# Kernel optimization log

Hardware: AMD Instinct MI355X
Metric: run time of the kernel (lower is better)

## Reference

```python
import jax, jax.numpy as jnp
import numpy as np

C = 1024
CI = 256  # in_channels // inter_ratio
BN_EPS = 1e-5


def setup_inputs() -> dict:
    key = jax.random.key(0)
    ks = jax.random.split(key, 12)
    B, H, W = 16, 64, 32
    xavier = lambda k, o, i: jax.random.uniform(k, (o, i), jnp.float32,
                                                -np.sqrt(6.0 / (o + i)), np.sqrt(6.0 / (o + i)))
    return {
        "x": jax.random.normal(ks[0], (B, C, H, W), jnp.float32),
        "theta_w": xavier(ks[1], CI, C), "theta_b": jnp.zeros((CI,), jnp.float32),
        "phi_w": xavier(ks[2], CI, C), "phi_b": jnp.zeros((CI,), jnp.float32),
        "g_w": xavier(ks[3], CI, C), "g_b": jnp.zeros((CI,), jnp.float32),
        "w_w": xavier(ks[4], C, CI), "w_b": jnp.zeros((C,), jnp.float32),
        # BatchNorm (inference-mode) params; random (not zero-init) so the block is non-trivial
        "bn_gamma": jax.random.normal(ks[5], (C,), jnp.float32) * 0.1 + 1.0,
        "bn_beta": jax.random.normal(ks[6], (C,), jnp.float32) * 0.1,
        "bn_mean": jax.random.normal(ks[7], (C,), jnp.float32) * 0.1,
        "bn_var": jax.random.uniform(ks[8], (C,), jnp.float32, 0.5, 1.5),
    }


def reference(x, theta_w, theta_b, phi_w, phi_b, g_w, g_b, w_w, w_b,
              bn_gamma, bn_beta, bn_mean, bn_var):
    B, Cc, H, W = x.shape
    N = H * W
    xf = x.reshape(B, Cc, N)  # [B, C, N]
    # 1x1 convs == channel GEMMs
    theta = jnp.einsum('oc,bcn->bno', theta_w, xf) + theta_b  # [B, N, Ci]
    phi = jnp.einsum('oc,bcn->bon', phi_w, xf) + phi_b[:, None]  # [B, Ci, N]
    g = jnp.einsum('oc,bcn->bno', g_w, xf) + g_b  # [B, N, Ci]
    attn = jax.nn.softmax(jnp.einsum('bno,bom->bnm', theta, phi), axis=-1)  # [B, N, N]
    y = jnp.einsum('bnm,bmo->bno', attn, g)  # [B, N, Ci]
    z = jnp.einsum('co,bno->bcn', w_w, y) + w_b[None, :, None]  # [B, C, N]
    inv = bn_gamma / jnp.sqrt(bn_var + BN_EPS)
    z = (z - bn_mean[None, :, None]) * inv[None, :, None] + bn_beta[None, :, None]
    return z.reshape(B, Cc, H, W) + x
```

## Files before the change

### kernel.cpp

```cpp
#include <hip/hip_runtime.h>
#include <cstdint>

#define BATCH 16
#define CH 1024
#define CIN 256
#define NSP 2048
#define BN_EPS 1e-5f

typedef _Float16 f16;
typedef f16   f16x8 __attribute__((ext_vector_type(8)));
typedef float f32x4 __attribute__((ext_vector_type(4)));

typedef __attribute__((address_space(3))) void lds_t;
typedef __attribute__((address_space(1))) const void gbl_t;

__device__ __forceinline__ void gld16(void* l, const void* g) {
    __builtin_amdgcn_global_load_lds((gbl_t*)g, (lds_t*)l, 16, 0, 0);
}

__global__ __launch_bounds__(256) void k_prep(
    const float* __restrict__ tw, const float* __restrict__ pw,
    const float* __restrict__ gw, const float* __restrict__ ww,
    const float* __restrict__ wb, const float* __restrict__ gamma,
    const float* __restrict__ beta, const float* __restrict__ mean,
    const float* __restrict__ var,
    f16* __restrict__ w_all, float* __restrict__ inv_out, float* __restrict__ off_out)
{
    int id = blockIdx.x * 256 + threadIdx.x;
    if (id < 4 * 262144) {
        int sel = id >> 18, off = id & 262143;
        const float* src = sel == 0 ? tw : sel == 1 ? pw : sel == 2 ? gw : ww;
        w_all[id] = (f16)src[off];
    } else {
        int c = id - 4 * 262144;
        if (c < CH) {
            float iv = gamma[c] * rsqrtf(var[c] + BN_EPS);
            inv_out[c] = iv;
            off_out[c] = (wb[c] - mean[c]) * iv + beta[c];
        }
    }
}

__global__ __launch_bounds__(256) void k_transpose_x(
    const float* __restrict__ x, f16* __restrict__ xT)
{
    __shared__ float tile[64 * 65];
    int t = threadIdx.x;
    int n0 = blockIdx.x * 64, c0 = blockIdx.y * 64, b = blockIdx.z;
    const float* xb = x + (size_t)b * CH * NSP;
    for (int k = 0; k < 4; ++k) {
        int id = t + 256 * k;
        int row = id >> 4, cc = id & 15;
        float4 v = *(const float4*)(xb + (size_t)(c0 + row) * NSP + n0 + cc * 4);
        tile[row * 65 + cc * 4 + 0] = v.x;
        tile[row * 65 + cc * 4 + 1] = v.y;
        tile[row * 65 + cc * 4 + 2] = v.z;
        tile[row * 65 + cc * 4 + 3] = v.w;
    }
    __syncthreads();
    f16* xTb = xT + (size_t)b * NSP * CH;
    for (int k = 0; k < 2; ++k) {
        int id = t + 256 * k;
        int n = id >> 3, c8 = id & 7;
        f16x8 o;
        #pragma unroll
        for (int j = 0; j < 8; ++j) o[j] = (f16)tile[(c8 * 8 + j) * 65 + n];
        *(f16x8*)(xTb + (size_t)(n0 + n) * CH + c0 + c8 * 8) = o;
    }
}

__global__ __launch_bounds__(256, 3) void k_qkv(
    const f16* __restrict__ xT, const f16* __restrict__ w_all,
    const float* __restrict__ tb, const float* __restrict__ pb,
    const float* __restrict__ gb,
    f16* __restrict__ theta, f16* __restrict__ phiT, f16* __restrict__ gT)
{
    __shared__ char smem[40960];
    f16* a_lds = (f16*)smem;
    f16* b_lds = (f16*)(smem + 8192);
    int t = threadIdx.x;
    int w = t >> 6, lane = t & 63, l15 = lane & 15, q = lane >> 4;
    int sw = l15 & 7;
    int n0 = blockIdx.x * 64, b = blockIdx.y, set = blockIdx.z;
    const f16* W  = w_all + (size_t)set * (CIN * CH);
    const f16* xA = xT + ((size_t)b * NSP + n0) * CH;

    int rA  = lane >> 3;
    int ccs = (lane & 7) ^ rA;

    f32x4 acc[4][4];
    #pragma unroll
    for (int i = 0; i < 4; ++i)
        #pragma unroll
        for (int j = 0; j < 4; ++j) acc[i][j] = (f32x4){0.f, 0.f, 0.f, 0.f};

    for (int it = 0; it < 16; ++it) {
        #pragma unroll
        for (int i = 0; i < 2; ++i) {
            int win = w * 2 + i;
            int n = win * 8 + rA;
            gld16((char*)a_lds + win * 1024,
                  xA + (size_t)n * CH + it * 64 + ccs * 8);
        }
        #pragma unroll
        for (int i = 0; i < 8; ++i) {
            int win = w * 8 + i;
            int o = win * 8 + rA;
            gld16((char*)b_lds + win * 1024,
                  W + (size_t)o * CH + it * 64 + ccs * 8);
        }
        __syncthreads();

        #pragma unroll
        for (int kl = 0; kl < 2; ++kl) {
            int c16 = kl * 4 + q;
            int pos = (c16 ^ sw) & 7;
            f16x8 af[4], bfr[4];
            #pragma unroll
            for (int tn = 0; tn < 4; ++tn)
                af[tn] = *(const f16x8*)(a_lds + (16 * tn + l15) * 64 + pos * 8);
            #pragma unroll
            for (int to = 0; to < 4; ++to)
                bfr[to] = *(const f16x8*)(b_lds + (64 * w + 16 * to + l15) * 64 + pos * 8);
            #pragma unroll
            for (int tn = 0; tn < 4; ++tn)
                #pragma unroll
                for (int to = 0; to < 4; ++to)
                    acc[tn][to] = __builtin_amdgcn_mfma_f32_16x16x32_f16(
                        af[tn], bfr[to], acc[tn][to], 0, 0, 0);
        }
        __syncthreads();
    }

    const float* bias = set == 0 ? tb : set == 1 ? pb : gb;
    float bv[4];
    #pragma unroll
    for (int to = 0; to < 4; ++to) bv[to] = bias[64 * w + 16 * to + l15];

    if (set < 2) {
        f16* e_lds = (f16*)smem;
        #pragma unroll
        for (int tn = 0; tn < 4; ++tn)
            #pragma unroll
            for (int to = 0; to < 4; ++to)
                #pragma unroll
                for (int r = 0; r < 4; ++r)
                    e_lds[(16 * tn + 4 * q + r) * 256 + 64 * w + 16 * to + l15] =
                        (f16)(acc[tn][to][r] + bv[to]);
        __syncthreads();
        f16* dst = (set == 0 ? theta : phiT) + ((size_t)b * NSP + n0) * CIN;
        for (int k2 = 0; k2 < 8; ++k2) {
            int id = t + 256 * k2;
            *(f16x8*)(dst + id * 8) = *(const f16x8*)(e_lds + id * 8);
        }
    } else {
        f16* e_lds = (f16*)smem;
        #pragma unroll
        for (int tn = 0; tn < 4; ++tn)
            #pragma unroll
            for (int to = 0; to < 4; ++to)
                #pragma unroll
                for (int r = 0; r < 4; ++r)
                    e_lds[(64 * w + 16 * to + l15) * 72 + 16 * tn + 4 * q + r] =
                        (f16)(acc[tn][to][r] + bv[to]);
        __syncthreads();
        f16* dst = gT + (size_t)b * CIN * NSP + n0;
        for (int k2 = 0; k2 < 8; ++k2) {
            int id = t + 256 * k2;
            int o = id >> 3, cc = id & 7;
            *(f16x8*)(dst + (size_t)o * NSP + cc * 8) = *(const f16x8*)(e_lds + o * 72 + cc * 8);
        }
    }
}

__global__ __launch_bounds__(256, 2) void k_attn(
    const f16* __restrict__ theta, const f16* __restrict__ phiT,
    const f16* __restrict__ gT, f16* __restrict__ y)
{
    __shared__ char smem[70656];
    f16* p_lds = (f16*)(smem + 65536);
    int t = threadIdx.x;
    int w = t >> 6, lane = t & 63, l15 = lane & 15, q = lane >> 4;
    int n0 = blockIdx.x * 64, b = blockIdx.y;

    f16x8 th[8];
    const f16* thp = theta + ((size_t)b * NSP + n0 + 16 * w + l15) * CIN + q * 8;
    #pragma unroll
    for (int kk = 0; kk < 8; ++kk) th[kk] = *(const f16x8*)(thp + kk * 32);

    f32x4 yacc[16];
    #pragma unroll
    for (int i = 0; i < 16; ++i) yacc[i] = (f32x4){0.f, 0.f, 0.f, 0.f};
    float m_run = -INFINITY, l_run = 0.f;

    const f16* phib = phiT + (size_t)b * NSP * CIN;
    const f16* gTb  = gT + (size_t)b * CIN * NSP;

    int prow_in = lane >> 5;
    int pchunk  = lane & 31;
    int grow_in = lane >> 2;
    int gslot   = lane & 3;

    auto stage = [&](int it, int bufsel) {
        char* pbuf = smem + bufsel * 16384;
        char* gbuf = smem + 32768 + bufsel * 16384;
        const f16* psrc = phib + (size_t)(it * 32) * CIN;
        #pragma unroll
        for (int i = 0; i < 4; ++i) {
            int win = w * 4 + i;
            int row = win * 2 + prow_in;
            int c = (pchunk & 24) | ((pchunk ^ row) & 7);
            gld16(pbuf + win * 1024, psrc + (size_t)row * CIN + c * 8);
        }
        #pragma unroll
        for (int i = 0; i < 4; ++i) {
            int win = w * 4 + i;
            int o = win * 16 + grow_in;
            int c = (gslot ^ o) & 3;
            gld16(gbuf + win * 1024, gTb + (size_t)o * NSP + it * 32 + c * 8);
        }
    };

    stage(0, 0);
    __syncthreads();

    for (int it = 0; it < 64; ++it) {
        int cur = it & 1;
        if (it < 63) stage(it + 1, cur ^ 1);
        const f16* phi_l = (const f16*)(smem + cur * 16384);
        const f16* g_l   = (const f16*)(smem + 32768 + cur * 16384);

        f32x4 sT[2];
        sT[0] = (f32x4){0.f, 0.f, 0.f, 0.f};
        sT[1] = (f32x4){0.f, 0.f, 0.f, 0.f};
        #pragma unroll
        for (int kk = 0; kk < 8; ++kk) {
            int c = kk * 4 + q;
            int pos = (c & 24) | ((c ^ (l15 & 7)) & 7);
            #pragma unroll
            for (int to = 0; to < 2; ++to) {
                f16x8 af = *(const f16x8*)(phi_l + (16 * to + l15) * 256 + pos * 8);
                sT[to] = __builtin_amdgcn_mfma_f32_16x16x32_f16(af, th[kk], sT[to], 0, 0, 0);
            }
        }

        float tm = fmaxf(
            fmaxf(fmaxf(sT[0][0], sT[0][1]), fmaxf(sT[0][2], sT[0][3])),
            fmaxf(fmaxf(sT[1][0], sT[1][1]), fmaxf(sT[1][2], sT[1][3])));
        tm = fmaxf(tm, __shfl_xor(tm, 16));
        tm = fmaxf(tm, __shfl_xor(tm, 32));
        float mnew  = fmaxf(m_run, tm);
        float alpha = __expf(m_run - mnew);
        float rs = 0.f;
        #pragma unroll
        for (int to = 0; to < 2; ++to)
            #pragma unroll
            for (int r = 0; r < 4; ++r) {
                float p = __expf(sT[to][r] - mnew);
                sT[to][r] = p;
                rs += p;
            }
        rs += __shfl_xor(rs, 16);
        rs += __shfl_xor(rs, 32);
        l_run = l_run * alpha + rs;
        m_run = mnew;

        #pragma unroll
        for (int to = 0; to < 2; ++to)
            #pragma unroll
            for (int r = 0; r < 4; ++r)
                p_lds[(16 * w + l15) * 40 + 16 * to + 4 * q + r] = (f16)sT[to][r];

        #pragma unroll
        for (int r = 0; r < 4; ++r) {
            float ar = __shfl(alpha, (lane & 48) | (4 * q + r));
            if (ar != 1.0f) {
                #pragma unroll
                for (int tco = 0; tco < 16; ++tco) yacc[tco][r] *= ar;
            }
        }

        f16x8 pa = *(const f16x8*)(p_lds + (16 * w + l15) * 40 + q * 8);
        int gpos = (q ^ (l15 & 3)) & 3;
        #pragma unroll
        for (int tco = 0; tco < 16; ++tco) {
            f16x8 gfr = *(const f16x8*)(g_l + (16 * tco + l15) * 32 + gpos * 8);
            yacc[tco] = __builtin_amdgcn_mfma_f32_16x16x32_f16(pa, gfr, yacc[tco], 0, 0, 0);
        }

        __syncthreads();
    }

    float linv = 1.0f / l_run;
    f16* e_lds = (f16*)smem;
    #pragma unroll
    for (int r = 0; r < 4; ++r) {
        float iv = __shfl(linv, (lane & 48) | (4 * q + r));
        #pragma unroll
        for (int tco = 0; tco < 16; ++tco)
            e_lds[(16 * w + 4 * q + r) * 256 + 16 * tco + l15] =
                (f16)(yacc[tco][r] * iv);
    }
    __syncthreads();
    f16* dst = y + ((size_t)b * NSP + n0) * CIN;
    for (int k2 = 0; k2 < 8; ++k2) {
        int id = t + 256 * k2;
        *(f16x8*)(dst + id * 8) = *(const f16x8*)(e_lds + id * 8);
    }
}

__global__ __launch_bounds__(256, 4) void k_out(
    const f16* __restrict__ yv, const f16* __restrict__ ww,
    const float* __restrict__ inv, const float* __restrict__ off,
    const float* __restrict__ x, float* __restrict__ out)
{
    __shared__ char smem[33792];
    f16*   y_lds = (f16*)smem;
    float* z_lds = (float*)smem;
    int t = threadIdx.x;
    int w = t >> 6, lane = t & 63, l15 = lane & 15, q = lane >> 4;
    int n0 = blockIdx.x * 64, c0 = blockIdx.y * 64, b = blockIdx.z;

    const f16* src = yv + ((size_t)b * NSP + n0) * CIN;
    for (int k2 = 0; k2 < 8; ++k2) {
        int id = t + 256 * k2;
        int n = id >> 5, cc = id & 31;
        *(f16x8*)(y_lds + n * 264 + cc * 8) = *(const f16x8*)(src + id * 8);
    }
    __syncthreads();

    f32x4 acc[4];
    #pragma unroll
    for (int i = 0; i < 4; ++i) acc[i] = (f32x4){0.f, 0.f, 0.f, 0.f};
    const f16* wp = ww + (size_t)c0 * CIN + q * 8;
    #pragma unroll
    for (int kk = 0; kk < 8; ++kk) {
        f16x8 bfr = *(const f16x8*)(y_lds + (16 * w + l15) * 264 + kk * 32 + q * 8);
        #pragma unroll
        for (int tc = 0; tc < 4; ++tc) {
            f16x8 af = *(const f16x8*)(wp + (size_t)(16 * tc + l15) * CIN + kk * 32);
            acc[tc] = __builtin_amdgcn_mfma_f32_16x16x32_f16(af, bfr, acc[tc], 0, 0, 0);
        }
    }

    __syncthreads();

    #pragma unroll
    for (int tc = 0; tc < 4; ++tc)
        #pragma unroll
        for (int r = 0; r < 4; ++r)
            z_lds[(16 * tc + 4 * q + r) * 68 + 16 * w + l15] = acc[tc][r];
    __syncthreads();

    #pragma unroll
    for (int k2 = 0; k2 < 4; ++k2) {
        int f  = t + 256 * k2;
        int cl = f >> 4, n4 = f & 15;
        int c  = c0 + cl;
        float4 z = *(const float4*)(z_lds + cl * 68 + n4 * 4);
        size_t idx = ((size_t)b * CH + c) * NSP + n0 + n4 * 4;
        float4 xv = *(const float4*)(x + idx);
        float iv = inv[c], ov = off[c];
        float4 o;
        o.x = z.x * iv + ov + xv.x;
        o.y = z.y * iv + ov + xv.y;
        o.z = z.z * iv + ov + xv.z;
        o.w = z.w * iv + ov + xv.w;
        *(float4*)(out + idx) = o;
    }
}

extern "C" void kernel_launch(void* const* d_in, const int* in_sizes, int n_in,
                              void* d_out, int out_size, void* d_ws, size_t ws_size,
                              hipStream_t stream)
{
    const float* x     = (const float*)d_in[0];
    const float* tw    = (const float*)d_in[1];
    const float* tb    = (const float*)d_in[2];
    const float* pw    = (const float*)d_in[3];
    const float* pb    = (const float*)d_in[4];
    const float* gw    = (const float*)d_in[5];
    const float* gb_   = (const float*)d_in[6];
    const float* ww    = (const float*)d_in[7];
    const float* wb    = (const float*)d_in[8];
    const float* gamma = (const float*)d_in[9];
    const float* beta  = (const float*)d_in[10];
    const float* mean  = (const float*)d_in[11];
    const float* var   = (const float*)d_in[12];
    float* out = (float*)d_out;

    char* ws = (char*)d_ws;
    f16* xT    = (f16*)ws;
    f16* theta = (f16*)(ws + 67108864);
    f16* phiT  = (f16*)(ws + 83886080);
    f16* gT    = (f16*)(ws + 100663296);
    f16* yv    = (f16*)(ws + 117440512);
    f16* w_all = (f16*)(ws + 134217728);
    float* inv  = (float*)(ws + 136314880);
    float* offv = (float*)(ws + 136318976);

    k_prep<<<4100, 256, 0, stream>>>(tw, pw, gw, ww, wb, gamma, beta, mean, var,
                                     w_all, inv, offv);
    k_transpose_x<<<dim3(32, 16, 16), 256, 0, stream>>>(x, xT);
    k_qkv<<<dim3(32, 16, 3), 256, 0, stream>>>(xT, w_all, tb, pb, gb_, theta, phiT, gT);
    k_attn<<<dim3(32, 16), 256, 0, stream>>>(theta, phiT, gT, yv);
    k_out<<<dim3(32, 16, 16), 256, 0, stream>>>(yv, w_all + 3 * 262144, inv, offv, x, out);
}
```

Measured before the change: 560.0 us.

## Retile output projection GEMM to 64x256 tiles with swizzled LDS staging

The output projection kernel now computes 256 output channels per block instead of 64, so each loaded y tile is reused four times more. Both y and weight tiles are staged into LDS through direct global-to-LDS loads with an XOR swizzle, in four K-steps. The epilogue is split into four passes, with residual x loads software-prefetched one pass ahead. In exchange, register pressure rises (launch bounds drop to 3 blocks per CU) and the grid shrinks to a quarter of the blocks.

```diff
diff --git a/kernel.cpp b/kernel.cpp
--- a/kernel.cpp
+++ b/kernel.cpp
@@ -309,64 +309,120 @@
     }
 }
 
-__global__ __launch_bounds__(256, 4) void k_out(
+__global__ __launch_bounds__(256, 3) void k_out(
     const f16* __restrict__ yv, const f16* __restrict__ ww,
     const float* __restrict__ inv, const float* __restrict__ off,
     const float* __restrict__ x, float* __restrict__ out)
 {
-    __shared__ char smem[33792];
-    f16*   y_lds = (f16*)smem;
+    __shared__ char smem[40960];
+    f16*   a_lds = (f16*)smem;
+    f16*   b_lds = (f16*)(smem + 8192);
     float* z_lds = (float*)smem;
     int t = threadIdx.x;
     int w = t >> 6, lane = t & 63, l15 = lane & 15, q = lane >> 4;
-    int n0 = blockIdx.x * 64, c0 = blockIdx.y * 64, b = blockIdx.z;
-
-    const f16* src = yv + ((size_t)b * NSP + n0) * CIN;
-    for (int k2 = 0; k2 < 8; ++k2) {
-        int id = t + 256 * k2;
-        int n = id >> 5, cc = id & 31;
-        *(f16x8*)(y_lds + n * 264 + cc * 8) = *(const f16x8*)(src + id * 8);
-    }
-    __syncthreads();
-
-    f32x4 acc[4];
-    #pragma unroll
-    for (int i = 0; i < 4; ++i) acc[i] = (f32x4){0.f, 0.f, 0.f, 0.f};
-    const f16* wp = ww + (size_t)c0 * CIN + q * 8;
-    #pragma unroll
-    for (int kk = 0; kk < 8; ++kk) {
-        f16x8 bfr = *(const f16x8*)(y_lds + (16 * w + l15) * 264 + kk * 32 + q * 8);
-        #pragma unroll
-        for (int tc = 0; tc < 4; ++tc) {
-            f16x8 af = *(const f16x8*)(wp + (size_t)(16 * tc + l15) * CIN + kk * 32);
-            acc[tc] = __builtin_amdgcn_mfma_f32_16x16x32_f16(af, bfr, acc[tc], 0, 0, 0);
-        }
-    }
-
-    __syncthreads();
-
-    #pragma unroll
-    for (int tc = 0; tc < 4; ++tc)
-        #pragma unroll
-        for (int r = 0; r < 4; ++r)
-            z_lds[(16 * tc + 4 * q + r) * 68 + 16 * w + l15] = acc[tc][r];
-    __syncthreads();
-
+    int sw = l15 & 7;
+    int n0 = blockIdx.x * 64, cb = blockIdx.y * 256, b = blockIdx.z;
+
+    const f16* yA = yv + ((size_t)b * NSP + n0) * CIN;
+    const f16* W  = ww + (size_t)cb * CIN;
+
+    int rA  = lane >> 3;
+    int ccs = (lane & 7) ^ rA;
+
+    f32x4 acc[4][4];
+    #pragma unroll
+    for (int i = 0; i < 4; ++i)
+        #pragma unroll
+        for (int j = 0; j < 4; ++j) acc[i][j] = (f32x4){0.f, 0.f, 0.f, 0.f};
+
+    for (int it = 0; it < 4; ++it) {
+        #pragma unroll
+        for (int i = 0; i < 2; ++i) {
+            int win = w * 2 + i;
+            int n = win * 8 + rA;
+            gld16((char*)a_lds + win * 1024,
+                  yA + (size_t)n * CIN + it * 64 + ccs * 8);
+        }
+        #pragma unroll
+        for (int i = 0; i < 8; ++i) {
+            int win = w * 8 + i;
+            int o = win * 8 + rA;
+            gld16((char*)b_lds + win * 1024,
+                  W + (size_t)o * CIN + it * 64 + ccs * 8);
+        }
+        __syncthreads();
+
+        #pragma unroll
+        for (int kl = 0; kl < 2; ++kl) {
+            int c16 = kl * 4 + q;
+            int pos = (c16 ^ sw) & 7;
+            f16x8 af[4], bfr[4];
+            #pragma unroll
+            for (int tn = 0; tn < 4; ++tn)
+                af[tn] = *(const f16x8*)(a_lds + (16 * tn + l15) * 64 + pos * 8);
+            #pragma unroll
+            for (int to = 0; to < 4; ++to)
+                bfr[to] = *(const f16x8*)(b_lds + (64 * w + 16 * to + l15) * 64 + pos * 8);
+            #pragma unroll
+            for (int tn = 0; tn < 4; ++tn)
+                #pragma unroll
+                for (int to = 0; to < 4; ++to)
+                    acc[tn][to] = __builtin_amdgcn_mfma_f32_16x16x32_f16(
+                        af[tn], bfr[to], acc[tn][to], 0, 0, 0);
+        }
+        __syncthreads();
+    }
+
+    float4 xv[4];
     #pragma unroll
     for (int k2 = 0; k2 < 4; ++k2) {
-        int f  = t + 256 * k2;
-        int cl = f >> 4, n4 = f & 15;
-        int c  = c0 + cl;
-        float4 z = *(const float4*)(z_lds + cl * 68 + n4 * 4);
-        size_t idx = ((size_t)b * CH + c) * NSP + n0 + n4 * 4;
-        float4 xv = *(const float4*)(x + idx);
-        float iv = inv[c], ov = off[c];
-        float4 o;
-        o.x = z.x * iv + ov + xv.x;
-        o.y = z.y * iv + ov + xv.y;
-        o.z = z.z * iv + ov + xv.z;
-        o.w = z.w * iv + ov + xv.w;
-        *(float4*)(out + idx) = o;
+        int f = t + 256 * k2;
+        int zrr = f >> 4, nn4 = f & 15;
+        int c = cb + 64 * (zrr >> 4) + (zrr & 15);
+        xv[k2] = *(const float4*)(x + ((size_t)b * CH + c) * NSP + n0 + nn4 * 4);
+    }
+
+    #pragma unroll
+    for (int to = 0; to < 4; ++to) {
+        #pragma unroll
+        for (int tn = 0; tn < 4; ++tn)
+            #pragma unroll
+            for (int r = 0; r < 4; ++r)
+                z_lds[(16 * w + l15) * 68 + 16 * tn + 4 * q + r] = acc[tn][to][r];
+        __syncthreads();
+
+        float4 nxt[4];
+        if (to < 3) {
+            #pragma unroll
+            for (int k2 = 0; k2 < 4; ++k2) {
+                int f = t + 256 * k2;
+                int zrr = f >> 4, nn4 = f & 15;
+                int c = cb + 64 * (zrr >> 4) + 16 * (to + 1) + (zrr & 15);
+                nxt[k2] = *(const float4*)(x + ((size_t)b * CH + c) * NSP + n0 + nn4 * 4);
+            }
+        }
+
+        #pragma unroll
+        for (int k2 = 0; k2 < 4; ++k2) {
+            int f = t + 256 * k2;
+            int zrr = f >> 4, nn4 = f & 15;
+            int c = cb + 64 * (zrr >> 4) + 16 * to + (zrr & 15);
+            float4 z = *(const float4*)(z_lds + zrr * 68 + nn4 * 4);
+            float iv = inv[c], ov = off[c];
+            size_t idx = ((size_t)b * CH + c) * NSP + n0 + nn4 * 4;
+            float4 o;
+            o.x = z.x * iv + ov + xv[k2].x;
+            o.y = z.y * iv + ov + xv[k2].y;
+            o.z = z.z * iv + ov + xv[k2].z;
+            o.w = z.w * iv + ov + xv[k2].w;
+            *(float4*)(out + idx) = o;
+        }
+
+        if (to < 3) {
+            #pragma unroll
+            for (int k2 = 0; k2 < 4; ++k2) xv[k2] = nxt[k2];
+            __syncthreads();
+        }
     }
 }
 
@@ -404,5 +460,5 @@
     k_transpose_x<<<dim3(32, 16, 16), 256, 0, stream>>>(x, xT);
     k_qkv<<<dim3(32, 16, 3), 256, 0, stream>>>(xT, w_all, tb, pb, gb_, theta, phiT, gT);
     k_attn<<<dim3(32, 16), 256, 0, stream>>>(theta, phiT, gT, yv);
-    k_out<<<dim3(32, 16, 16), 256, 0, stream>>>(yv, w_all + 3 * 262144, inv, offv, x, out);
-}
+    k_out<<<dim3(32, 4, 16), 256, 0, stream>>>(yv, w_all + 3 * 262144, inv, offv, x, out);
+}
```

New measurement: 483.8 us. -13.6%, faster.
